# Kernel tuning notes

Measured on AMD Instinct MI355X. Metric: run time of the kernel, lower is better.

## Reference

```python
import jax, jax.numpy as jnp
import numpy as np
from jax import lax

# 8-bit symmetric quantization: clip bound = 2**(prec-1) - 1
CLIP = 127.0
EPS = 1e-6  # epsilon in scale denominator to avoid div-by-zero (mirrors QuantOps bound epsilon)


def setup_inputs() -> dict:
    key = jax.random.key(0)
    k1, k2 = jax.random.split(key)
    B, CIN, COUT = 8192, 4096, 8192
    act = jax.random.normal(k1, (B, CIN), dtype=jnp.float32)
    w = jax.random.normal(k2, (CIN, COUT), dtype=jnp.float32)
    return {"act": act, "w": w}


def reference(act, w):
    # --- activation quantization: per-input-channel symmetric scale, shape (1, Cin) ---
    act_bound = jnp.max(jnp.abs(act), axis=0, keepdims=True) + EPS     # (1, Cin)
    act_scale = CLIP / act_bound                                        # (1, Cin)
    act_q = jnp.clip(jnp.round(act * act_scale), -CLIP, CLIP)           # int values in fp32

    # fold inverse activation scale into weight rows: w_scaled_rows = (1/act_scale) * w
    w_scaled = w * (1.0 / act_scale).reshape(-1, 1)                     # (Cin, Cout)

    # --- weight quantization: per-output-channel symmetric scale, shape (1, Cout) ---
    w_bound = jnp.max(jnp.abs(w_scaled), axis=0, keepdims=True) + EPS   # (1, Cout)
    w_scale = CLIP / w_bound                                            # (1, Cout)
    w_q = jnp.clip(jnp.round(w_scaled * w_scale), -CLIP, CLIP)

    out_i32 = lax.dot_general(
        act_q.astype(jnp.int8),
        w_q.astype(jnp.int8),
        dimension_numbers=(((1,), (0,)), ((), ())),
        preferred_element_type=jnp.int32,
    )
    out = out_i32.astype(jnp.float32)

    # inline dequant by per-output-channel weight scale (act scale already folded into w)
    return (out * (1.0 / w_scale)).astype(jnp.float32)
```

## Files before the change

### kernel.cpp

```cpp
#include <hip/hip_runtime.h>
#include <hip/hip_bf16.h>
#include <stdint.h>

#define BDIM 8192
#define CIN  4096
#define COUT 8192
#define EPSQ 1e-6f

typedef int v4i __attribute__((ext_vector_type(4)));

#define GLD16_TO_LDS(gp, lp)                                                   \
    __builtin_amdgcn_global_load_lds(                                          \
        (const __attribute__((address_space(1))) void*)(gp),                   \
        (__attribute__((address_space(3))) void*)(lp), 16, 0, 0)

__device__ __forceinline__ int q8i(float x) {
    float r = rintf(x);
    r = fminf(127.0f, fmaxf(-127.0f, r));
    return (int)r;
}

__global__ void act_absmax_kernel(const float* __restrict__ act,
                                  int* __restrict__ amax_bits) {
    int c4 = (blockIdx.x << 8) + threadIdx.x;
    int r0 = blockIdx.y << 7;
    const float4* p = (const float4*)act + (size_t)r0 * (CIN / 4) + c4;
    float mx = 0.f, my = 0.f, mz = 0.f, mw = 0.f;
#pragma unroll 4
    for (int r = 0; r < 128; ++r) {
        float4 v = p[(size_t)r * (CIN / 4)];
        mx = fmaxf(mx, fabsf(v.x));
        my = fmaxf(my, fabsf(v.y));
        mz = fmaxf(mz, fabsf(v.z));
        mw = fmaxf(mw, fabsf(v.w));
    }
    int c = c4 << 2;
    atomicMax(amax_bits + c + 0, __float_as_int(mx));
    atomicMax(amax_bits + c + 1, __float_as_int(my));
    atomicMax(amax_bits + c + 2, __float_as_int(mz));
    atomicMax(amax_bits + c + 3, __float_as_int(mw));
}

__global__ void act_quant_kernel(const float4* __restrict__ act4,
                                 const int4* __restrict__ amax_bits4,
                                 float* __restrict__ inv_as,
                                 int* __restrict__ actq_packed) {
    int flat4 = blockIdx.x * 256 + threadIdx.x;
    int c4 = flat4 & ((CIN / 4) - 1);
    float4 v = act4[flat4];
    int4 mb = amax_bits4[c4];
    float sx = 127.0f / (__int_as_float(mb.x) + EPSQ);
    float sy = 127.0f / (__int_as_float(mb.y) + EPSQ);
    float sz = 127.0f / (__int_as_float(mb.z) + EPSQ);
    float sw = 127.0f / (__int_as_float(mb.w) + EPSQ);
    int q0 = q8i(v.x * sx), q1 = q8i(v.y * sy), q2 = q8i(v.z * sz), q3 = q8i(v.w * sw);
    int packed = (q0 & 0xff) | ((q1 & 0xff) << 8) | ((q2 & 0xff) << 16) | ((q3 & 0xff) << 24);
    actq_packed[flat4] = packed;
    if (flat4 < CIN / 4) {
        int c = c4 << 2;
        inv_as[c + 0] = 1.0f / sx;
        inv_as[c + 1] = 1.0f / sy;
        inv_as[c + 2] = 1.0f / sz;
        inv_as[c + 3] = 1.0f / sw;
    }
}

__global__ void w_absmax_kernel(const float* __restrict__ w,
                                const float* __restrict__ inv_as,
                                int* __restrict__ wmax_bits) {
    int c4 = (blockIdx.x << 8) + threadIdx.x;
    int k0 = blockIdx.y << 6;
    const float4* p = (const float4*)w + (size_t)k0 * (COUT / 4) + c4;
    float mx = 0.f, my = 0.f, mz = 0.f, mw = 0.f;
#pragma unroll 4
    for (int r = 0; r < 64; ++r) {
        float ia = inv_as[k0 + r];
        float4 v = p[(size_t)r * (COUT / 4)];
        mx = fmaxf(mx, fabsf(v.x * ia));
        my = fmaxf(my, fabsf(v.y * ia));
        mz = fmaxf(mz, fabsf(v.z * ia));
        mw = fmaxf(mw, fabsf(v.w * ia));
    }
    int c = c4 << 2;
    atomicMax(wmax_bits + c + 0, __float_as_int(mx));
    atomicMax(wmax_bits + c + 1, __float_as_int(my));
    atomicMax(wmax_bits + c + 2, __float_as_int(mz));
    atomicMax(wmax_bits + c + 3, __float_as_int(mw));
}

__global__ void w_quant_t_kernel(const float* __restrict__ w,
                                 const float* __restrict__ inv_as,
                                 const int* __restrict__ wmax_bits,
                                 signed char* __restrict__ wqT) {
    __shared__ int tile32[16][65];
    int t = threadIdx.x;
    int k0 = blockIdx.x << 6;
    int j0 = blockIdx.y << 6;
    int tx = t & 63;
    int ty = t >> 6;
    int j = j0 + tx;
    float wscale = 127.0f / (__int_as_float(wmax_bits[j]) + EPSQ);
#pragma unroll
    for (int r = 0; r < 4; ++r) {
        int a = r * 4 + ty;
        int kb = k0 + (a << 2);
        int packed = 0;
#pragma unroll
        for (int u = 0; u < 4; ++u) {
            int k = kb + u;
            float wsc = w[(size_t)k * COUT + j] * inv_as[k];
            int q = q8i(wsc * wscale);
            packed |= (q & 0xff) << (8 * u);
        }
        tile32[a][tx] = packed;
    }
    __syncthreads();
    int j_loc = t >> 2;
    int c = t & 3;
    int4 v;
    v.x = tile32[c * 4 + 0][j_loc];
    v.y = tile32[c * 4 + 1][j_loc];
    v.z = tile32[c * 4 + 2][j_loc];
    v.w = tile32[c * 4 + 3][j_loc];
    *(int4*)(wqT + (size_t)(j0 + j_loc) * CIN + k0 + c * 16) = v;
}

__global__ __launch_bounds__(256) void gemm_i8_kernel(
    const signed char* __restrict__ Aq,
    const signed char* __restrict__ Bq,
    const int* __restrict__ wmax_bits,
    float* __restrict__ out) {
    __shared__ __align__(16) signed char As[128 * 64];
    __shared__ __align__(16) signed char Bs[128 * 64];

    const int tid = threadIdx.x;
    const int wave = tid >> 6;
    const int lane = tid & 63;
    const int bm = blockIdx.y << 7;
    const int bn = blockIdx.x << 7;
    const int wm = (wave >> 1) << 6;
    const int wn = (wave & 1) << 6;

    const int g = lane >> 4;
    const int l16 = lane & 15;

    v4i acc[4][4] = {};

    for (int kt = 0; kt < CIN; kt += 64) {
        __syncthreads();
#pragma unroll
        for (int t = 0; t < 2; ++t) {
            int c0 = (wave * 2 + t) * 64;
            int mm = (t << 6) + lane;
            int gg = wave;
            const signed char* ga = Aq + ((size_t)(bm + mm) << 12) + kt + (gg << 4);
            GLD16_TO_LDS(ga, As + (c0 << 4));
            const signed char* gb = Bq + ((size_t)(bn + mm) << 12) + kt + (gg << 4);
            GLD16_TO_LDS(gb, Bs + (c0 << 4));
        }
        __syncthreads();

        v4i af[4], bf[4];
#pragma unroll
        for (int t = 0; t < 4; ++t)
            af[t] = *(const v4i*)(As + (((g << 7) + wm + (t << 4) + l16) << 4));
#pragma unroll
        for (int t = 0; t < 4; ++t)
            bf[t] = *(const v4i*)(Bs + (((g << 7) + wn + (t << 4) + l16) << 4));

#pragma unroll
        for (int tm = 0; tm < 4; ++tm)
#pragma unroll
            for (int tn = 0; tn < 4; ++tn)
                acc[tm][tn] = __builtin_amdgcn_mfma_i32_16x16x64_i8(
                    af[tm], bf[tn], acc[tm][tn], 0, 0, 0);
    }

#pragma unroll
    for (int tn = 0; tn < 4; ++tn) {
        int col = bn + wn + (tn << 4) + l16;
        float wscale = 127.0f / (__int_as_float(wmax_bits[col]) + EPSQ);
        float invws = 1.0f / wscale;
#pragma unroll
        for (int tm = 0; tm < 4; ++tm) {
            int row0 = bm + wm + (tm << 4) + (g << 2);
#pragma unroll
            for (int r = 0; r < 4; ++r)
                out[((size_t)(row0 + r) << 13) + col] = (float)acc[tm][tn][r] * invws;
        }
    }
}

extern "C" void kernel_launch(void* const* d_in, const int* in_sizes, int n_in,
                              void* d_out, int out_size, void* d_ws, size_t ws_size,
                              hipStream_t stream) {
    const float* act = (const float*)d_in[0];
    const float* w   = (const float*)d_in[1];
    float* out = (float*)d_out;
    char* ws = (char*)d_ws;

    int*   amax_bits = (int*)ws;
    float* inv_as    = (float*)(ws + 16384);
    int*   wmax_bits = (int*)(ws + 32768);
    signed char* actq = (signed char*)(ws + 65536);
    signed char* wqT  = (signed char*)(ws + 65536 + (size_t)BDIM * CIN);

    act_absmax_kernel<<<dim3(4, 64), 256, 0, stream>>>(act, amax_bits);
    act_quant_kernel<<<(BDIM * CIN / 4) / 256, 256, 0, stream>>>(
        (const float4*)act, (const int4*)amax_bits, inv_as, (int*)actq);
    w_absmax_kernel<<<dim3(8, 64), 256, 0, stream>>>(w, inv_as, wmax_bits);
    w_quant_t_kernel<<<dim3(64, 128), 256, 0, stream>>>(w, inv_as, wmax_bits, wqT);
    gemm_i8_kernel<<<dim3(COUT / 128, BDIM / 128), 256, 0, stream>>>(
        actq, wqT, wmax_bits, out);
}
```

Baseline: 986.8 us.

## Rewrite int8 GEMM with 256x256 tiles, 4-stage LDS pipeline and block swizzle

The int8 GEMM moves from 128x128 tiles with 256 threads and a single-buffered LDS load to 256x256 tiles with 512 threads and a 4-stage ring buffer in 128KB of LDS. Global-to-LDS loads are issued three stages ahead and gated by explicit vmcnt waits, and MFMA blocks get raised priority. Block indices are swizzled so neighbouring blocks share operand rows and columns in cache. The absmax reduction kernels also get twice as many blocks to add parallelism. The cost is heavy register and LDS use (one block per CU) and fragile hand-written wait counts.

After: 924.2 us. 1.07x faster.

```diff
diff --git a/kernel.cpp b/kernel.cpp
--- a/kernel.cpp
+++ b/kernel.cpp
@@ -23,11 +23,11 @@
 __global__ void act_absmax_kernel(const float* __restrict__ act,
                                   int* __restrict__ amax_bits) {
     int c4 = (blockIdx.x << 8) + threadIdx.x;
-    int r0 = blockIdx.y << 7;
+    int r0 = blockIdx.y << 6;
     const float4* p = (const float4*)act + (size_t)r0 * (CIN / 4) + c4;
     float mx = 0.f, my = 0.f, mz = 0.f, mw = 0.f;
 #pragma unroll 4
-    for (int r = 0; r < 128; ++r) {
+    for (int r = 0; r < 64; ++r) {
         float4 v = p[(size_t)r * (CIN / 4)];
         mx = fmaxf(mx, fabsf(v.x));
         my = fmaxf(my, fabsf(v.y));
@@ -69,11 +69,11 @@
                                 const float* __restrict__ inv_as,
                                 int* __restrict__ wmax_bits) {
     int c4 = (blockIdx.x << 8) + threadIdx.x;
-    int k0 = blockIdx.y << 6;
+    int k0 = blockIdx.y << 5;
     const float4* p = (const float4*)w + (size_t)k0 * (COUT / 4) + c4;
     float mx = 0.f, my = 0.f, mz = 0.f, mw = 0.f;
 #pragma unroll 4
-    for (int r = 0; r < 64; ++r) {
+    for (int r = 0; r < 32; ++r) {
         float ia = inv_as[k0 + r];
         float4 v = p[(size_t)r * (COUT / 4)];
         mx = fmaxf(mx, fabsf(v.x * ia));
@@ -125,65 +125,111 @@
     *(int4*)(wqT + (size_t)(j0 + j_loc) * CIN + k0 + c * 16) = v;
 }
 
-__global__ __launch_bounds__(256) void gemm_i8_kernel(
+__global__ __launch_bounds__(512, 2) void gemm_i8_kernel(
     const signed char* __restrict__ Aq,
     const signed char* __restrict__ Bq,
     const int* __restrict__ wmax_bits,
     float* __restrict__ out) {
-    __shared__ __align__(16) signed char As[128 * 64];
-    __shared__ __align__(16) signed char Bs[128 * 64];
+    __shared__ __align__(16) signed char lds[131072];
+    signed char* As = lds;
+    signed char* Bs = lds + 65536;
 
     const int tid = threadIdx.x;
     const int wave = tid >> 6;
     const int lane = tid & 63;
-    const int bm = blockIdx.y << 7;
-    const int bn = blockIdx.x << 7;
-    const int wm = (wave >> 1) << 6;
-    const int wn = (wave & 1) << 6;
-
     const int g = lane >> 4;
     const int l16 = lane & 15;
 
-    v4i acc[4][4] = {};
-
-    for (int kt = 0; kt < CIN; kt += 64) {
-        __syncthreads();
-#pragma unroll
-        for (int t = 0; t < 2; ++t) {
-            int c0 = (wave * 2 + t) * 64;
-            int mm = (t << 6) + lane;
-            int gg = wave;
-            const signed char* ga = Aq + ((size_t)(bm + mm) << 12) + kt + (gg << 4);
-            GLD16_TO_LDS(ga, As + (c0 << 4));
-            const signed char* gb = Bq + ((size_t)(bn + mm) << 12) + kt + (gg << 4);
-            GLD16_TO_LDS(gb, Bs + (c0 << 4));
-        }
-        __syncthreads();
-
-        v4i af[4], bf[4];
-#pragma unroll
-        for (int t = 0; t < 4; ++t)
-            af[t] = *(const v4i*)(As + (((g << 7) + wm + (t << 4) + l16) << 4));
-#pragma unroll
-        for (int t = 0; t < 4; ++t)
-            bf[t] = *(const v4i*)(Bs + (((g << 7) + wn + (t << 4) + l16) << 4));
-
-#pragma unroll
-        for (int tm = 0; tm < 4; ++tm)
-#pragma unroll
-            for (int tn = 0; tn < 4; ++tn)
-                acc[tm][tn] = __builtin_amdgcn_mfma_i32_16x16x64_i8(
-                    af[tm], bf[tn], acc[tm][tn], 0, 0, 0);
-    }
+    const int bid = blockIdx.x;
+    const int swz = (bid & 7) * 128 + (bid >> 3);
+    const int bm = (swz >> 5) << 8;
+    const int bn = (swz & 31) << 8;
+
+    const int wm128 = (wave >> 2) << 7;
+    const int wn64 = (wave & 3) << 6;
+
+    const int m = tid & 255;
+    const int gq = tid >> 8;
+    const signed char* aP = Aq + ((size_t)(bm + m) << 12) + (gq << 4);
+    const signed char* bP = Bq + ((size_t)(bn + m) << 12) + (gq << 4);
+    const int ldsOff = tid << 4;
+
+    const int offA = ((g << 8) + wm128 + l16) << 4;
+    const int offB = ((g << 8) + wn64 + l16) << 4;
+
+    v4i acc[8][4] = {};
+
+#define STAGE_STEP(t_)                                                         \
+    do {                                                                       \
+        signed char* As_ = As + (((t_) & 3) << 14);                            \
+        signed char* Bs_ = Bs + (((t_) & 3) << 14);                            \
+        const int kb_ = (t_) << 6;                                             \
+        GLD16_TO_LDS(aP + kb_,      As_ + ldsOff);                             \
+        GLD16_TO_LDS(aP + kb_ + 32, As_ + 8192 + ldsOff);                      \
+        GLD16_TO_LDS(bP + kb_,      Bs_ + ldsOff);                             \
+        GLD16_TO_LDS(bP + kb_ + 32, Bs_ + 8192 + ldsOff);                      \
+    } while (0)
+
+#define COMPUTE_STEP(s_)                                                       \
+    do {                                                                       \
+        const signed char* Ab_ = As + (((s_) & 3) << 14);                      \
+        const signed char* Bb_ = Bs + (((s_) & 3) << 14);                      \
+        v4i af_[8], bf_[4];                                                    \
+        _Pragma("unroll")                                                      \
+        for (int t = 0; t < 8; ++t)                                            \
+            af_[t] = *(const v4i*)(Ab_ + offA + (t << 8));                     \
+        _Pragma("unroll")                                                      \
+        for (int t = 0; t < 4; ++t)                                            \
+            bf_[t] = *(const v4i*)(Bb_ + offB + (t << 8));                     \
+        __builtin_amdgcn_s_setprio(1);                                         \
+        _Pragma("unroll")                                                      \
+        for (int tm = 0; tm < 8; ++tm)                                         \
+            _Pragma("unroll")                                                  \
+            for (int tn = 0; tn < 4; ++tn)                                     \
+                acc[tm][tn] = __builtin_amdgcn_mfma_i32_16x16x64_i8(           \
+                    af_[tm], bf_[tn], acc[tm][tn], 0, 0, 0);                   \
+        __builtin_amdgcn_s_setprio(0);                                         \
+    } while (0)
+
+    STAGE_STEP(0);
+    STAGE_STEP(1);
+    STAGE_STEP(2);
+    asm volatile("s_waitcnt vmcnt(8)" ::: "memory");
+
+#pragma unroll 1
+    for (int s = 0; s < 61; ++s) {
+        __builtin_amdgcn_s_barrier();
+        __builtin_amdgcn_sched_barrier(0);
+        STAGE_STEP(s + 3);
+        COMPUTE_STEP(s);
+        asm volatile("s_waitcnt vmcnt(8)" ::: "memory");
+        __builtin_amdgcn_sched_barrier(0);
+    }
+    __builtin_amdgcn_s_barrier();
+    __builtin_amdgcn_sched_barrier(0);
+    COMPUTE_STEP(61);
+    asm volatile("s_waitcnt vmcnt(4)" ::: "memory");
+    __builtin_amdgcn_sched_barrier(0);
+    __builtin_amdgcn_s_barrier();
+    __builtin_amdgcn_sched_barrier(0);
+    COMPUTE_STEP(62);
+    asm volatile("s_waitcnt vmcnt(0)" ::: "memory");
+    __builtin_amdgcn_sched_barrier(0);
+    __builtin_amdgcn_s_barrier();
+    __builtin_amdgcn_sched_barrier(0);
+    COMPUTE_STEP(63);
+
+#undef STAGE_STEP
+#undef COMPUTE_STEP
 
 #pragma unroll
     for (int tn = 0; tn < 4; ++tn) {
-        int col = bn + wn + (tn << 4) + l16;
+        int col = bn + wn64 + (tn << 4) + l16;
         float wscale = 127.0f / (__int_as_float(wmax_bits[col]) + EPSQ);
         float invws = 1.0f / wscale;
 #pragma unroll
-        for (int tm = 0; tm < 4; ++tm) {
-            int row0 = bm + wm + (tm << 4) + (g << 2);
+        for (int tm = 0; tm < 8; ++tm) {
+            int row0 = bm + wm128 + (tm << 4) + (g << 2);
 #pragma unroll
             for (int r = 0; r < 4; ++r)
                 out[((size_t)(row0 + r) << 13) + col] = (float)acc[tm][tn][r] * invws;
@@ -205,11 +251,11 @@
     signed char* actq = (signed char*)(ws + 65536);
     signed char* wqT  = (signed char*)(ws + 65536 + (size_t)BDIM * CIN);
 
-    act_absmax_kernel<<<dim3(4, 64), 256, 0, stream>>>(act, amax_bits);
+    act_absmax_kernel<<<dim3(4, 128), 256, 0, stream>>>(act, amax_bits);
     act_quant_kernel<<<(BDIM * CIN / 4) / 256, 256, 0, stream>>>(
         (const float4*)act, (const int4*)amax_bits, inv_as, (int*)actq);
-    w_absmax_kernel<<<dim3(8, 64), 256, 0, stream>>>(w, inv_as, wmax_bits);
+    w_absmax_kernel<<<dim3(8, 128), 256, 0, stream>>>(w, inv_as, wmax_bits);
     w_quant_t_kernel<<<dim3(64, 128), 256, 0, stream>>>(w, inv_as, wmax_bits, wqT);
-    gemm_i8_kernel<<<dim3(COUT / 128, BDIM / 128), 256, 0, stream>>>(
+    gemm_i8_kernel<<<COUT / 256 * (BDIM / 256), 512, 0, stream>>>(
         actq, wqT, wmax_bits, out);
 }
```
